# Kernel optimization log

Hardware: AMD Instinct MI355X
Metric: run time of the kernel (lower is better)

The kernel has to match this reference:

```python
import jax, jax.numpy as jnp
import numpy as np

KERNEL_SIZE = 11
OUT_CH = 512
IN_CH = 512


def make_pos_grid(k):
    # centered integer offsets, grid flattened at the end: shape (2, k*k)
    coords = jnp.arange(k, dtype=jnp.float32) - (k - 1) / 2.0
    yy, xx = jnp.meshgrid(coords, coords, indexing="ij")
    return jnp.stack([yy.reshape(-1), xx.reshape(-1)], axis=0)  # (2, k*k)


def setup_inputs() -> dict:
    key = jax.random.key(0)
    k1, _ = jax.random.split(key)
    # raw Cholesky parameters per (out_channel, in_channel) pair; diagonal goes
    # through exp() in reference() to guarantee positive-definite covariances.
    chol_raw = 0.1 * jax.random.normal(k1, (OUT_CH, IN_CH, 2, 2), dtype=jnp.float32)
    pos_grid = make_pos_grid(KERNEL_SIZE)
    return {"chol_raw": chol_raw, "pos_grid": pos_grid}


def reference(chol_raw, pos_grid):
    # chol_raw: (O, I, 2, 2) raw params; pos_grid: (2, K) with K = k*k
    O, I = chol_raw.shape[0], chol_raw.shape[1]
    K = pos_grid.shape[-1]
    k = int(round(np.sqrt(K)))

    # Lower-triangular Cholesky factor with positive diagonal:
    # L = [[exp(a), 0], [c, exp(d)]]
    l11 = jnp.exp(chol_raw[..., 0, 0])[..., None]  # (O, I, 1)
    l21 = chol_raw[..., 1, 0][..., None]           # (O, I, 1)
    l22 = jnp.exp(chol_raw[..., 1, 1])[..., None]  # (O, I, 1)

    x1 = pos_grid[0]  # (K,)
    x2 = pos_grid[1]  # (K,)

    # Inlined forward substitution: solve L b = x for each (o, i, position)
    b1 = x1 / l11                    # (O, I, K)
    b2 = (x2 - l21 * b1) / l22       # (O, I, K)

    # dists = sum over the 2-vector of squares = x^T S^{-1} x
    dists = (b1 * b1 + b2 * b2).reshape((O, I, k, k))
    return dists
```

## Files before the change

kernel.cpp:

```cpp
#include <hip/hip_runtime.h>

#define KK 121
#define OUT_CH 512
#define IN_CH 512
#define NPAIR (OUT_CH * IN_CH)
#define NOUT (NPAIR * KK)
#define NVEC (NOUT / 4)

__global__ __launch_bounds__(256) void
quad_multi2d_kernel(const float* __restrict__ chol,
                    const float* __restrict__ pg,
                    float* __restrict__ out) {
    __shared__ float s_x1[KK];
    __shared__ float s_x2[KK];
    {
        int t = threadIdx.x;
        if (t < KK) {
            s_x1[t] = pg[t];
            s_x2[t] = pg[KK + t];
        }
    }
    __syncthreads();

    int tid = blockIdx.x * blockDim.x + threadIdx.x;
    if (tid >= NVEC) return;

    int e0   = tid * 4;
    int pair = e0 / KK;
    int kp   = e0 - pair * KK;

    float4 cp  = ((const float4*)chol)[pair];
    float  e1  = __expf(-cp.x);
    float  l21 = cp.z;
    float  e2  = __expf(-cp.w);

    float r[4];
#pragma unroll
    for (int j = 0; j < 4; ++j) {
        if (kp == KK) {
            kp = 0;
            ++pair;
            cp  = ((const float4*)chol)[pair];
            e1  = __expf(-cp.x);
            l21 = cp.z;
            e2  = __expf(-cp.w);
        }
        float b1 = s_x1[kp] * e1;
        float b2 = (s_x2[kp] - l21 * b1) * e2;
        r[j] = b1 * b1 + b2 * b2;
        ++kp;
    }

    float4 o;
    o.x = r[0]; o.y = r[1]; o.z = r[2]; o.w = r[3];
    ((float4*)out)[tid] = o;
}

extern "C" void kernel_launch(void* const* d_in, const int* in_sizes, int n_in,
                              void* d_out, int out_size, void* d_ws, size_t ws_size,
                              hipStream_t stream) {
    const float* chol = (const float*)d_in[0];
    const float* pg   = (const float*)d_in[1];
    float* out        = (float*)d_out;

    const int block = 256;
    const int grid  = (NVEC + block - 1) / block;
    quad_multi2d_kernel<<<grid, block, 0, stream>>>(chol, pg, out);
}
```

Measured before the change: 158.3 us.

## Precompute per-pair parameters in a prep kernel and make the main loop branch-free

Adds a prep kernel that computes exp-transformed Cholesky factors once per pair into workspace. The main kernel then loads two precomputed pair records and selects between them without a branch. Shared-memory grid copies are replicated 8 times with padding so that lanes in a wave read different banks. A fused fallback runs when the workspace is too small; the cost is an extra kernel launch plus a workspace round trip. Since the kernel is bound by writing its output, the gain is uncertain.

```diff
diff --git a/kernel.cpp b/kernel.cpp
--- a/kernel.cpp
+++ b/kernel.cpp
@@ -1,58 +1,110 @@
 #include <hip/hip_runtime.h>
 
 #define KK 121
-#define OUT_CH 512
-#define IN_CH 512
-#define NPAIR (OUT_CH * IN_CH)
+#define NPAIR (512 * 512)
 #define NOUT (NPAIR * KK)
 #define NVEC (NOUT / 4)
+#define WSREQ ((size_t)(NPAIR + 1) * 16)
 
 __global__ __launch_bounds__(256) void
-quad_multi2d_kernel(const float* __restrict__ chol,
-                    const float* __restrict__ pg,
-                    float* __restrict__ out) {
-    __shared__ float s_x1[KK];
-    __shared__ float s_x2[KK];
-    {
-        int t = threadIdx.x;
-        if (t < KK) {
-            s_x1[t] = pg[t];
-            s_x2[t] = pg[KK + t];
-        }
+prep_params_kernel(const float* __restrict__ chol, float4* __restrict__ q) {
+    int tid = blockIdx.x * 256 + threadIdx.x;
+    if (tid < NPAIR) {
+        float4 c = ((const float4*)chol)[tid];
+        float e1 = __expf(-c.x);
+        float e2 = __expf(-c.w);
+        float4 o;
+        o.x = e1; o.y = c.z * e2; o.z = e2; o.w = 0.f;
+        q[tid] = o;
+    } else if (tid == NPAIR) {
+        q[tid] = make_float4(0.f, 0.f, 0.f, 0.f);
+    }
+}
+
+__global__ __launch_bounds__(256) void
+quad_main_kernel(const float4* __restrict__ q, const float* __restrict__ pg,
+                 float4* __restrict__ out) {
+    __shared__ float sx1[8 * 129];
+    __shared__ float sx2[8 * 129];
+    int t = threadIdx.x;
+    if (t < KK) {
+        float a = pg[t], b = pg[KK + t];
+#pragma unroll
+        for (int r = 0; r < 8; ++r) { sx1[r * 129 + t] = a; sx2[r * 129 + t] = b; }
     }
     __syncthreads();
 
-    int tid = blockIdx.x * blockDim.x + threadIdx.x;
-    if (tid >= NVEC) return;
-
+    int tid  = blockIdx.x * 256 + t;
     int e0   = tid * 4;
     int pair = e0 / KK;
-    int kp   = e0 - pair * KK;
+    int kp0  = e0 - pair * KK;
 
-    float4 cp  = ((const float4*)chol)[pair];
-    float  e1  = __expf(-cp.x);
-    float  l21 = cp.z;
-    float  e2  = __expf(-cp.w);
+    float4 q0 = q[pair];
+    float4 q1 = q[pair + 1];
+    int rb = ((t & 63) >> 3) * 129;
 
-    float r[4];
+    float res[4];
 #pragma unroll
     for (int j = 0; j < 4; ++j) {
-        if (kp == KK) {
-            kp = 0;
-            ++pair;
-            cp  = ((const float4*)chol)[pair];
-            e1  = __expf(-cp.x);
-            l21 = cp.z;
-            e2  = __expf(-cp.w);
-        }
-        float b1 = s_x1[kp] * e1;
-        float b2 = (s_x2[kp] - l21 * b1) * e2;
-        r[j] = b1 * b1 + b2 * b2;
-        ++kp;
+        int  kp = kp0 + j;
+        bool w  = kp >= KK;
+        kp = w ? kp - KK : kp;
+        float e1 = w ? q1.x : q0.x;
+        float f  = w ? q1.y : q0.y;
+        float e2 = w ? q1.z : q0.z;
+        float x1 = sx1[rb + kp];
+        float x2 = sx2[rb + kp];
+        float b1 = x1 * e1;
+        float b2 = fmaf(-f, b1, x2 * e2);
+        res[j] = fmaf(b2, b2, b1 * b1);
     }
+    float4 o;
+    o.x = res[0]; o.y = res[1]; o.z = res[2]; o.w = res[3];
+    out[tid] = o;
+}
 
+__global__ __launch_bounds__(256) void
+quad_fused_kernel(const float* __restrict__ chol, const float* __restrict__ pg,
+                  float* __restrict__ out) {
+    __shared__ float sx1[8 * 129];
+    __shared__ float sx2[8 * 129];
+    int t = threadIdx.x;
+    if (t < KK) {
+        float a = pg[t], b = pg[KK + t];
+#pragma unroll
+        for (int r = 0; r < 8; ++r) { sx1[r * 129 + t] = a; sx2[r * 129 + t] = b; }
+    }
+    __syncthreads();
+
+    int tid  = blockIdx.x * 256 + t;
+    int e0   = tid * 4;
+    int pair = e0 / KK;
+    int kp0  = e0 - pair * KK;
+    int pairB = pair + 1 < NPAIR ? pair + 1 : NPAIR - 1;
+
+    float4 cA = ((const float4*)chol)[pair];
+    float4 cB = ((const float4*)chol)[pairB];
+    float e1A = __expf(-cA.x), e2A = __expf(-cA.w), fA = cA.z * e2A;
+    float e1B = __expf(-cB.x), e2B = __expf(-cB.w), fB = cB.z * e2B;
+    int rb = ((t & 63) >> 3) * 129;
+
+    float res[4];
+#pragma unroll
+    for (int j = 0; j < 4; ++j) {
+        int  kp = kp0 + j;
+        bool w  = kp >= KK;
+        kp = w ? kp - KK : kp;
+        float e1 = w ? e1B : e1A;
+        float f  = w ? fB  : fA;
+        float e2 = w ? e2B : e2A;
+        float x1 = sx1[rb + kp];
+        float x2 = sx2[rb + kp];
+        float b1 = x1 * e1;
+        float b2 = fmaf(-f, b1, x2 * e2);
+        res[j] = fmaf(b2, b2, b1 * b1);
+    }
     float4 o;
-    o.x = r[0]; o.y = r[1]; o.z = r[2]; o.w = r[3];
+    o.x = res[0]; o.y = res[1]; o.z = res[2]; o.w = res[3];
     ((float4*)out)[tid] = o;
 }
 
@@ -64,6 +116,14 @@
     float* out        = (float*)d_out;
 
     const int block = 256;
-    const int grid  = (NVEC + block - 1) / block;
-    quad_multi2d_kernel<<<grid, block, 0, stream>>>(chol, pg, out);
+    const int gridMain = NVEC / block;
+
+    if (ws_size >= WSREQ) {
+        float4* q = (float4*)d_ws;
+        const int gridPrep = (NPAIR + 1 + block - 1) / block;
+        prep_params_kernel<<<gridPrep, block, 0, stream>>>(chol, q);
+        quad_main_kernel<<<gridMain, block, 0, stream>>>(q, pg, (float4*)out);
+    } else {
+        quad_fused_kernel<<<gridMain, block, 0, stream>>>(chol, pg, out);
+    }
 }
```

Measured after the change: 136.1 us. 14.0% less time.

## Rewrite quadratic form as rank-3 combination and stage outputs in shared memory

Applied to the files above, without the earlier changes.

Expands the distance into P*x1^2 + Q*x2^2 + R*x1*x2 with per-pair coefficients computed once, so each output costs two FMAs and a multiply, and removes the per-element pair division and boundary branch. Each block handles 64 pairs, writes results into a shared staging buffer, and then streams them out as coalesced float4 stores. This adds about 31 KB of shared memory per block and an extra barrier, which may limit occupancy on what is a store-bandwidth-bound kernel. The algebraic expansion can also change floating-point rounding slightly.

```diff
diff --git a/kernel.cpp b/kernel.cpp
--- a/kernel.cpp
+++ b/kernel.cpp
@@ -1,69 +1,66 @@
 #include <hip/hip_runtime.h>
 
 #define KK 121
-#define OUT_CH 512
-#define IN_CH 512
-#define NPAIR (OUT_CH * IN_CH)
-#define NOUT (NPAIR * KK)
-#define NVEC (NOUT / 4)
+#define NPAIR (512 * 512)
+#define PPB 64
+#define NBLK (NPAIR / PPB)
+#define STAGE_F4 (PPB * KK / 4)
 
 __global__ __launch_bounds__(256) void
-quad_multi2d_kernel(const float* __restrict__ chol,
-                    const float* __restrict__ pg,
-                    float* __restrict__ out) {
-    __shared__ float s_x1[KK];
-    __shared__ float s_x2[KK];
-    {
-        int t = threadIdx.x;
-        if (t < KK) {
-            s_x1[t] = pg[t];
-            s_x2[t] = pg[KK + t];
-        }
+quad_rank3_kernel(const float4* __restrict__ chol4,
+                  const float* __restrict__ pg,
+                  float4* __restrict__ out4) {
+    __shared__ float4 s_uvw[KK];
+    __shared__ __align__(16) float stage[PPB * KK];
+
+    const int t = threadIdx.x;
+
+    if (t < KK) {
+        float x1 = pg[t];
+        float x2 = pg[KK + t];
+        float4 g;
+        g.x = x1 * x1; g.y = x2 * x2; g.z = x1 * x2; g.w = 0.f;
+        s_uvw[t] = g;
     }
+
+    const int p       = t & 63;
+    const int quarter = t >> 6;
+    const int k0 = (quarter == 0) ? 0 : (30 * quarter + 1);
+    const int k1 = (quarter == 0) ? 31 : (k0 + 30);
+
+    float4 c = chol4[blockIdx.x * PPB + p];
+    float e1 = __expf(-c.x);
+    float e2 = __expf(-c.w);
+    float f  = c.z * e2;
+    float P  = e1 * e1 * fmaf(f, f, 1.f);
+    float Q  = e2 * e2;
+    float R  = -2.f * f * e1 * e2;
+
     __syncthreads();
 
-    int tid = blockIdx.x * blockDim.x + threadIdx.x;
-    if (tid >= NVEC) return;
-
-    int e0   = tid * 4;
-    int pair = e0 / KK;
-    int kp   = e0 - pair * KK;
-
-    float4 cp  = ((const float4*)chol)[pair];
-    float  e1  = __expf(-cp.x);
-    float  l21 = cp.z;
-    float  e2  = __expf(-cp.w);
-
-    float r[4];
-#pragma unroll
-    for (int j = 0; j < 4; ++j) {
-        if (kp == KK) {
-            kp = 0;
-            ++pair;
-            cp  = ((const float4*)chol)[pair];
-            e1  = __expf(-cp.x);
-            l21 = cp.z;
-            e2  = __expf(-cp.w);
-        }
-        float b1 = s_x1[kp] * e1;
-        float b2 = (s_x2[kp] - l21 * b1) * e2;
-        r[j] = b1 * b1 + b2 * b2;
-        ++kp;
+    float* st = &stage[p * KK];
+#pragma unroll 5
+    for (int k = k0; k < k1; ++k) {
+        float4 g = s_uvw[k];
+        st[k] = fmaf(P, g.x, fmaf(Q, g.y, R * g.z));
     }
 
-    float4 o;
-    o.x = r[0]; o.y = r[1]; o.z = r[2]; o.w = r[3];
-    ((float4*)out)[tid] = o;
+    __syncthreads();
+
+    const float4* s4 = (const float4*)stage;
+    float4* o = out4 + (size_t)blockIdx.x * STAGE_F4;
+#pragma unroll
+    for (int i = t; i < STAGE_F4; i += 256) {
+        o[i] = s4[i];
+    }
 }
 
 extern "C" void kernel_launch(void* const* d_in, const int* in_sizes, int n_in,
                               void* d_out, int out_size, void* d_ws, size_t ws_size,
                               hipStream_t stream) {
-    const float* chol = (const float*)d_in[0];
-    const float* pg   = (const float*)d_in[1];
-    float* out        = (float*)d_out;
+    const float4* chol4 = (const float4*)d_in[0];
+    const float* pg     = (const float*)d_in[1];
+    float4* out4        = (float4*)d_out;
 
-    const int block = 256;
-    const int grid  = (NVEC + block - 1) / block;
-    quad_multi2d_kernel<<<grid, block, 0, stream>>>(chol, pg, out);
+    quad_rank3_kernel<<<NBLK, 256, 0, stream>>>(chol4, pg, out4);
 }
```

New measurement: 131.6 us. -16.8%, faster.
